# Kernel tuning notes

Measured on AMD Instinct MI355X. Metric: run time of the kernel, lower is better.

## Reference

```python
import jax, jax.numpy as jnp
import numpy as np
from jax import lax

EPS = 1e-8  # torch CosineSimilarity eps
TAU = 0.5   # temperature

def _l2norm(v):
    # clamp norm like torch.nn.CosineSimilarity
    n = jnp.sqrt(jnp.sum(v * v, axis=-1, keepdims=True))
    return v / jnp.maximum(n, EPS)

def setup_inputs() -> dict:
    key = jax.random.key(0)
    k1, k2, k3, k4 = jax.random.split(key, 4)
    B, C, H, W = 64, 3, 384, 384
    hidden, size, L = 768, 16, 1024
    x = jax.random.normal(k1, (B, C, H, W), dtype=jnp.float32)
    conv_w = jax.random.normal(k2, (hidden, C, size, size), dtype=jnp.float32) * 0.02
    conv_b = jax.random.normal(k3, (hidden,), dtype=jnp.float32) * 0.02
    latent = jax.random.normal(k4, (1, L, hidden), dtype=jnp.float32)
    return {"x": x, "conv_w": conv_w, "conv_b": conv_b, "latent": latent}

def reference(x, conv_w, conv_b, latent):
    B = x.shape[0]
    stride = conv_w.shape[-1]
    # patch embedding: Conv2d stride=kernel (non-overlapping patches)
    patch = lax.conv_general_dilated(
        x, conv_w, window_strides=(stride, stride), padding='VALID',
        dimension_numbers=('NCHW', 'OIHW', 'NCHW')) + conv_b[None, :, None, None]
    D = patch.shape[1]
    patch = patch.reshape(B, D, -1).transpose(0, 2, 1)  # (B, N, D)
    N = patch.shape[1]
    pn = _l2norm(patch)                                  # (B, N, D)
    # all-pairs cosine similarity via GEMM on normalized vectors
    SIM = jnp.einsum('bnd,bmd->bnm', pn, pn)             # (B, N, N)
    off_diag = 1.0 - jnp.eye(N, dtype=SIM.dtype)
    far_sum = jnp.sum(jnp.exp(SIM / TAU) * off_diag, axis=(1, 2))  # (B,)
    # patch vs latent cosine similarity
    ln = _l2norm(latent[0])                              # (L, D)
    close = jnp.einsum('bnd,ld->bnl', pn, ln)            # (B, N, L)
    close_sum = jnp.sum(jnp.exp(close / TAU), axis=(1, 2))  # (B,)
    loss = -jnp.log(close_sum / far_sum)
    return jnp.mean(loss)
```

## Files before the change

kernel.cpp:

```cpp
#include <hip/hip_runtime.h>
#include <hip/hip_bf16.h>
#include <hip/hip_fp8.h>

#define KDIM   768
#define NPATCH 576
#define NPAD   640
#define NBATCH 64
#define MROWS  36864
#define LROWS  1024

typedef __attribute__((ext_vector_type(8))) int int8v;
typedef __attribute__((ext_vector_type(4))) int int4v;
typedef __attribute__((ext_vector_type(4))) float float4v;
typedef unsigned char u8;

__device__ inline u8 f2fp8(float f) { __hip_fp8_e4m3 t(f); return (u8)t.__x; }

__device__ __forceinline__ void gload_lds16(const u8* g, u8* l) {
    __builtin_amdgcn_global_load_lds(
        (const __attribute__((address_space(1))) unsigned int*)g,
        (__attribute__((address_space(3))) unsigned int*)l, 16, 0, 0);
}

__device__ __forceinline__ void ds_read_b256(unsigned addr, int4v& lo, int4v& hi) {
    asm volatile("ds_read_b128 %0, %2\n\tds_read_b128 %1, %2 offset:16"
                 : "=&v"(lo), "=&v"(hi) : "v"(addr));
}

__global__ __launch_bounds__(256) void im2col_cast_v(const float* __restrict__ x,
                                                     u8* __restrict__ A) {
    int t = blockIdx.x * 256 + threadIdx.x;
    int row = t / 48;
    int ci = t - row * 48;
    int c = ci >> 4, i = ci & 15;
    int b = row / NPATCH;
    int p = row - b * NPATCH;
    int ph = p / 24, pw = p - ph * 24;
    const float* src = x + (((size_t)b * 3 + c) * 384 + ph * 16 + i) * 384 + pw * 16;
    float4v f[4];
#pragma unroll
    for (int q = 0; q < 4; q++) f[q] = *(const float4v*)(src + q * 4);
    unsigned int o[4];
#pragma unroll
    for (int q = 0; q < 4; q++) {
        o[q] = 0;
#pragma unroll
        for (int e = 0; e < 4; e++) o[q] |= ((unsigned int)f2fp8(f[q][e])) << (8 * e);
    }
    *(int4v*)(A + (size_t)row * KDIM + c * 256 + i * 16) = *(int4v*)o;
}

__global__ __launch_bounds__(256) void cast_w(const float* __restrict__ src,
                                              u8* __restrict__ dst) {
    int t = blockIdx.x * 256 + threadIdx.x;
    const float* s = src + (size_t)t * 16;
    unsigned int o[4];
#pragma unroll
    for (int q = 0; q < 4; q++) {
        float4v f = *(const float4v*)(s + q * 4);
        o[q] = 0;
#pragma unroll
        for (int e = 0; e < 4; e++) o[q] |= ((unsigned int)f2fp8(f[e] * 32.0f)) << (8 * e);
    }
    *(int4v*)(dst + (size_t)t * 16) = *(int4v*)o;
}

__global__ __launch_bounds__(256) void normalize_latent(const float* __restrict__ src,
                                                        u8* __restrict__ dst) {
    int wave = threadIdx.x >> 6, lane = threadIdx.x & 63;
    int row = blockIdx.x * 4 + wave;
    const float4v* pr = (const float4v*)(src + (size_t)row * KDIM);
    float4v v[3];
    float ss = 0.f;
#pragma unroll
    for (int c = 0; c < 3; c++) {
        v[c] = pr[lane + 64 * c];
#pragma unroll
        for (int e = 0; e < 4; e++) ss += v[c][e] * v[c][e];
    }
#pragma unroll
    for (int off = 32; off; off >>= 1) ss += __shfl_xor(ss, off);
    float scale = 16.0f / fmaxf(sqrtf(ss), 1e-8f);
#pragma unroll
    for (int c = 0; c < 3; c++) {
        unsigned int o = 0;
#pragma unroll
        for (int e = 0; e < 4; e++) o |= ((unsigned int)f2fp8(v[c][e] * scale)) << (8 * e);
        *(unsigned int*)(dst + (size_t)row * KDIM + c * 256 + lane * 4) = o;
    }
}

__global__ __launch_bounds__(256) void inv_norm(const float* __restrict__ rssq,
                                                float* __restrict__ rn) {
    int t = blockIdx.x * 256 + threadIdx.x;
    int p = t % NPAD;
    rn[t] = (p < NPATCH) ? (1.0f / fmaxf(sqrtf(rssq[t]), 1e-8f)) : 0.0f;
}

__device__ __forceinline__ void gemm_mainloop_fp8(const u8* __restrict__ Ab,
                                                  const u8* __restrict__ Bb,
                                                  u8* As, u8* Bs,
                                                  float4v acc[4][4], int sA, int sB) {
    int tid = threadIdx.x;
    int lane = tid & 63;
    int wu = __builtin_amdgcn_readfirstlane(tid >> 6);
    int quad = lane >> 4, l15 = lane & 15;
    int wm = wu & 1, wn = wu >> 1;
    int lr = lane >> 3, ls = lane & 7;
    int gs = ((((ls >> 1) - lr) & 3) << 1) | (ls & 1);
    int gvoff = lr * KDIM + gs * 16;
    const u8* gAu = Ab + (size_t)(wu * 32) * KDIM;
    const u8* gBu = Bb + (size_t)(wu * 32) * KDIM;
    int woffL = wu * 32 * 128;
    int lg = ((quad + (l15 & 3)) & 3) * 32;
    unsigned asb = (unsigned)(size_t)As + (unsigned)((wm * 64 + l15) * 128 + lg);
    unsigned bsb = (unsigned)(size_t)Bs + (unsigned)((wn * 64 + l15) * 128 + lg);

#pragma unroll
    for (int i = 0; i < 4; i++) {
        gload_lds16(gAu + i * 8 * KDIM + gvoff, As + woffL + i * 1024);
        gload_lds16(gBu + i * 8 * KDIM + gvoff, Bs + woffL + i * 1024);
    }
#pragma unroll 1
    for (int t = 0; t < 6; t++) {
        int cur = (t & 1) * 16384;
        if (t < 5) {
            int nxt = ((t + 1) & 1) * 16384;
            int ks = (t + 1) * 128;
#pragma unroll
            for (int i = 0; i < 4; i++) {
                gload_lds16(gAu + ks + i * 8 * KDIM + gvoff, As + nxt + woffL + i * 1024);
                gload_lds16(gBu + ks + i * 8 * KDIM + gvoff, Bs + nxt + woffL + i * 1024);
            }
            asm volatile("s_waitcnt vmcnt(8)" ::: "memory");
        } else {
            asm volatile("s_waitcnt vmcnt(0)" ::: "memory");
        }
        __builtin_amdgcn_s_barrier();
        asm volatile("" ::: "memory");
        int4v al[4], ah[4], bl[4], bh[4];
#pragma unroll
        for (int j = 0; j < 4; j++) ds_read_b256(bsb + cur + j * 2048, bl[j], bh[j]);
#pragma unroll
        for (int i = 0; i < 4; i++) ds_read_b256(asb + cur + i * 2048, al[i], ah[i]);
        asm volatile("s_waitcnt lgkmcnt(8)"
                     : "+v"(bl[0]), "+v"(bl[1]), "+v"(bl[2]), "+v"(bl[3]),
                       "+v"(bh[0]), "+v"(bh[1]), "+v"(bh[2]), "+v"(bh[3]));
        int8v b[4];
#pragma unroll
        for (int j = 0; j < 4; j++)
            b[j] = __builtin_shufflevector(bl[j], bh[j], 0, 1, 2, 3, 4, 5, 6, 7);
        asm volatile("s_waitcnt lgkmcnt(0)"
                     : "+v"(al[0]), "+v"(al[1]), "+v"(al[2]), "+v"(al[3]),
                       "+v"(ah[0]), "+v"(ah[1]), "+v"(ah[2]), "+v"(ah[3]));
        int8v a[4];
#pragma unroll
        for (int i = 0; i < 4; i++)
            a[i] = __builtin_shufflevector(al[i], ah[i], 0, 1, 2, 3, 4, 5, 6, 7);
        __builtin_amdgcn_sched_barrier(0);
        __builtin_amdgcn_s_barrier();
        asm volatile("" ::: "memory");
        __builtin_amdgcn_s_setprio(1);
#pragma unroll
        for (int i = 0; i < 4; i++)
#pragma unroll
            for (int j = 0; j < 4; j++)
                acc[i][j] = __builtin_amdgcn_mfma_scale_f32_16x16x128_f8f6f4(
                    a[i], b[j], acc[i][j], 0, 0, 0, sA, 0, sB);
        __builtin_amdgcn_s_setprio(0);
    }
}

__device__ __forceinline__ float block_reduce_sum(float s, float* red) {
#pragma unroll
    for (int off = 32; off; off >>= 1) s += __shfl_down(s, off);
    int wave = threadIdx.x >> 6, lane = threadIdx.x & 63;
    if (lane == 0) red[wave] = s;
    __syncthreads();
    return red[0] + red[1] + red[2] + red[3];
}

__global__ __launch_bounds__(256) void gemm_conv(const u8* __restrict__ A,
                                                 const u8* __restrict__ Wm,
                                                 const float* __restrict__ bias,
                                                 u8* __restrict__ pn,
                                                 float* __restrict__ rssq) {
    __shared__ u8 As[2 * 128 * 128], Bs[2 * 128 * 128];
    int xcd = blockIdx.x & 7, q = blockIdx.x >> 3;
    int mb = xcd * 36 + q / 6;
    int nb = q % 6;
    int wave = threadIdx.x >> 6, lane = threadIdx.x & 63;
    int quad = lane >> 4, l15 = lane & 15;
    int wm = wave & 1, wn = wave >> 1;
    float4v acc[4][4] = {};
    gemm_mainloop_fp8(A + (size_t)mb * 128 * KDIM, Wm + (size_t)nb * 128 * KDIM,
                      As, Bs, acc, 0x7F7F7F7F, 0x7A7A7A7A);
    float bv[4];
#pragma unroll
    for (int j = 0; j < 4; j++) bv[j] = bias[nb * 128 + wn * 64 + j * 16 + l15];
#pragma unroll
    for (int i = 0; i < 4; i++) {
#pragma unroll
        for (int r = 0; r < 4; r++) {
            int row = mb * 128 + wm * 64 + i * 16 + quad * 4 + r;
            int b = row / NPATCH;
            int prow = row + b * 64;
            float ssq = 0.f;
#pragma unroll
            for (int j = 0; j < 4; j++) {
                int col = nb * 128 + wn * 64 + j * 16 + l15;
                float v = acc[i][j][r] + bv[j];
                ssq += v * v;
                pn[(size_t)prow * KDIM + col] = f2fp8(v * 16.0f);
            }
#pragma unroll
            for (int off = 1; off < 16; off <<= 1) ssq += __shfl_xor(ssq, off);
            if (l15 == 0) atomicAdd(&rssq[prow], ssq);
        }
    }
}

__global__ __launch_bounds__(256) void gemm_scores(const u8* __restrict__ pn,
                                                   const u8* __restrict__ Lm,
                                                   const float* __restrict__ rn,
                                                   float* __restrict__ far_sum,
                                                   float* __restrict__ close_sum) {
    __shared__ u8 As[2 * 128 * 128], Bs[2 * 128 * 128];
    __shared__ float red[4];
    int wave = threadIdx.x >> 6, lane = threadIdx.x & 63;
    int quad = lane >> 4, l15 = lane & 15;
    int wm = wave & 1, wn = wave >> 1;
    float4v acc[4][4] = {};

    if (blockIdx.x < 2560) {
        int xcd = blockIdx.x & 7, q = blockIdx.x >> 3;
        int mb = xcd * 40 + (q >> 3);
        int nb = q & 7;
        gemm_mainloop_fp8(pn + (size_t)mb * 128 * KDIM, Lm + (size_t)nb * 128 * KDIM,
                          As, Bs, acc, 0x7B7B7B7B, 0x7B7B7B7B);
        int batch = mb / 5;
        int ptile = (mb - batch * 5) * 128;
        float s = 0.f;
#pragma unroll
        for (int i = 0; i < 4; i++) {
#pragma unroll
            for (int r = 0; r < 4; r++) {
                int p = ptile + wm * 64 + i * 16 + quad * 4 + r;
                if (p < NPATCH) {
                    float rrow = rn[batch * NPAD + p];
#pragma unroll
                    for (int j = 0; j < 4; j++) s += __expf(2.0f * acc[i][j][r] * rrow);
                }
            }
        }
        float tot = block_reduce_sum(s, red);
        if (threadIdx.x == 0) atomicAdd(&close_sum[batch], tot);
    } else {
        int sbid = blockIdx.x - 2560;
        int xcd = sbid & 7, q = sbid >> 3;
        int b = xcd * 8 + q / 15;
        int t = q % 15;
        int mt, nt;
        if (t < 5) { mt = t; nt = t; }
        else {
            int u = t - 5;
            mt = (u < 4) ? 0 : (u < 7) ? 1 : (u < 9) ? 2 : 3;
            nt = (u < 4) ? u + 1 : (u < 7) ? u - 2 : (u < 9) ? u - 5 : 4;
        }
        const u8* base = pn + (size_t)b * NPAD * KDIM;
        gemm_mainloop_fp8(base + (size_t)mt * 128 * KDIM, base + (size_t)nt * 128 * KDIM,
                          As, Bs, acc, 0x7B7B7B7B, 0x7B7B7B7B);
        const float* rnb = rn + b * NPAD;
        float rcol[4];
#pragma unroll
        for (int j = 0; j < 4; j++) rcol[j] = rnb[nt * 128 + wn * 64 + j * 16 + l15];
        float s = 0.f;
#pragma unroll
        for (int i = 0; i < 4; i++) {
#pragma unroll
            for (int r = 0; r < 4; r++) {
                int row = mt * 128 + wm * 64 + i * 16 + quad * 4 + r;
                if (row < NPATCH) {
                    float rrow = rnb[row];
#pragma unroll
                    for (int j = 0; j < 4; j++) {
                        int col = nt * 128 + wn * 64 + j * 16 + l15;
                        if (col < NPATCH && row != col)
                            s += __expf(2.0f * acc[i][j][r] * rrow * rcol[j]);
                    }
                }
            }
        }
        if (mt != nt) s *= 2.0f;
        float tot = block_reduce_sum(s, red);
        if (threadIdx.x == 0) atomicAdd(&far_sum[b], tot);
    }
}

__global__ void loss_kernel(const float* __restrict__ far_sum,
                            const float* __restrict__ close_sum,
                            float* __restrict__ out) {
    int t = threadIdx.x;
    float v = logf(far_sum[t]) - logf(close_sum[t]);
#pragma unroll
    for (int off = 32; off; off >>= 1) v += __shfl_xor(v, off);
    if (t == 0) out[0] = v * (1.0f / 64.0f);
}

extern "C" void kernel_launch(void* const* d_in, const int* in_sizes, int n_in,
                              void* d_out, int out_size, void* d_ws, size_t ws_size,
                              hipStream_t stream) {
    const float* x      = (const float*)d_in[0];
    const float* conv_w = (const float*)d_in[1];
    const float* conv_b = (const float*)d_in[2];
    const float* latent = (const float*)d_in[3];
    float* out = (float*)d_out;
    char* ws = (char*)d_ws;

    u8* pn = (u8*)ws;
    u8* A  = (u8*)(ws + 31457280);
    u8* Wm = (u8*)(ws + 59768832);
    u8* Lm = (u8*)(ws + 60358656);
    float* rssq = (float*)(ws + 61145088);
    float* sums = (float*)(ws + 61308928);
    float* rn   = (float*)(ws + 31457280);
    float* far_sum = sums;
    float* close_sum = sums + 64;

    hipMemsetAsync(rssq, 0, (40960 + 128) * sizeof(float), stream);
    im2col_cast_v<<<36864 * 48 / 256, 256, 0, stream>>>(x, A);
    cast_w<<<144, 256, 0, stream>>>(conv_w, Wm);
    normalize_latent<<<LROWS / 4, 256, 0, stream>>>(latent, Lm);

    gemm_conv<<<288 * 6, 256, 0, stream>>>(A, Wm, conv_b, pn, rssq);
    inv_norm<<<160, 256, 0, stream>>>(rssq, rn);

    gemm_scores<<<2560 + 960, 256, 0, stream>>>(pn, Lm, rn, far_sum, close_sum);

    loss_kernel<<<1, 64, 0, stream>>>(far_sum, close_sum, out);
}
```

Before: 291.4 us.

## Widen GEMM tiles to 128x256 with 512-thread blocks and new LDS swizzle

Both FP8 GEMM kernels move from 128x128 tiles on 256 threads to 128x256 tiles on 512 threads. Each A tile is now reused across twice as many output columns, which cuts global and LDS traffic per FLOP. The LDS swizzle is changed to an 8-way 16-byte pattern with separate low and high read addresses. The far-sum tiling now enumerates upper-triangular 128x256 tiles per batch, weighting each half-tile by 0, 1 or 2. This adds more LDS per block and more complex tile indexing, and may lower occupancy.

After: 311.7 us. 6.9% more time.

```diff
diff --git a/kernel.cpp b/kernel.cpp
--- a/kernel.cpp
+++ b/kernel.cpp
@@ -22,10 +22,8 @@
         (__attribute__((address_space(3))) unsigned int*)l, 16, 0, 0);
 }
 
-__device__ __forceinline__ void ds_read_b256(unsigned addr, int4v& lo, int4v& hi) {
-    asm volatile("ds_read_b128 %0, %2\n\tds_read_b128 %1, %2 offset:16"
-                 : "=&v"(lo), "=&v"(hi) : "v"(addr));
-}
+#define DSR(dst, areg, imm) \
+    asm volatile("ds_read_b128 %0, %1 offset:" #imm : "=&v"(dst) : "v"(areg))
 
 __global__ __launch_bounds__(256) void im2col_cast_v(const float* __restrict__ x,
                                                      u8* __restrict__ A) {
@@ -107,42 +105,57 @@
     int quad = lane >> 4, l15 = lane & 15;
     int wm = wu & 1, wn = wu >> 1;
     int lr = lane >> 3, ls = lane & 7;
-    int gs = ((((ls >> 1) - lr) & 3) << 1) | (ls & 1);
+    int gs = (ls - lr) & 7;
     int gvoff = lr * KDIM + gs * 16;
-    const u8* gAu = Ab + (size_t)(wu * 32) * KDIM;
+    const u8* gAu = Ab + (size_t)(wu * 16) * KDIM;
     const u8* gBu = Bb + (size_t)(wu * 32) * KDIM;
-    int woffL = wu * 32 * 128;
-    int lg = ((quad + (l15 & 3)) & 3) * 32;
-    unsigned asb = (unsigned)(size_t)As + (unsigned)((wm * 64 + l15) * 128 + lg);
-    unsigned bsb = (unsigned)(size_t)Bs + (unsigned)((wn * 64 + l15) * 128 + lg);
-
-#pragma unroll
-    for (int i = 0; i < 4; i++) {
-        gload_lds16(gAu + i * 8 * KDIM + gvoff, As + woffL + i * 1024);
-        gload_lds16(gBu + i * 8 * KDIM + gvoff, Bs + woffL + i * 1024);
-    }
+    int woffA = wu * 16 * 128;
+    int woffB = wu * 32 * 128;
+    int pl = ((2 * quad) + (l15 & 7)) & 7;
+    int ph = ((2 * quad + 1) + (l15 & 7)) & 7;
+    unsigned asbL = (unsigned)(size_t)As + (unsigned)((wm * 64 + l15) * 128 + pl * 16);
+    unsigned asbH = (unsigned)(size_t)As + (unsigned)((wm * 64 + l15) * 128 + ph * 16);
+    unsigned bsbL = (unsigned)(size_t)Bs + (unsigned)((wn * 64 + l15) * 128 + pl * 16);
+    unsigned bsbH = (unsigned)(size_t)Bs + (unsigned)((wn * 64 + l15) * 128 + ph * 16);
+
+#pragma unroll
+    for (int i = 0; i < 2; i++)
+        gload_lds16(gAu + i * 8 * KDIM + gvoff, As + woffA + i * 1024);
+#pragma unroll
+    for (int i = 0; i < 4; i++)
+        gload_lds16(gBu + i * 8 * KDIM + gvoff, Bs + woffB + i * 1024);
+
 #pragma unroll 1
     for (int t = 0; t < 6; t++) {
-        int cur = (t & 1) * 16384;
+        int curA = (t & 1) * 16384;
+        int curB = (t & 1) * 32768;
         if (t < 5) {
-            int nxt = ((t + 1) & 1) * 16384;
+            int nxtA = ((t + 1) & 1) * 16384;
+            int nxtB = ((t + 1) & 1) * 32768;
             int ks = (t + 1) * 128;
 #pragma unroll
-            for (int i = 0; i < 4; i++) {
-                gload_lds16(gAu + ks + i * 8 * KDIM + gvoff, As + nxt + woffL + i * 1024);
-                gload_lds16(gBu + ks + i * 8 * KDIM + gvoff, Bs + nxt + woffL + i * 1024);
-            }
-            asm volatile("s_waitcnt vmcnt(8)" ::: "memory");
+            for (int i = 0; i < 2; i++)
+                gload_lds16(gAu + ks + i * 8 * KDIM + gvoff, As + nxtA + woffA + i * 1024);
+#pragma unroll
+            for (int i = 0; i < 4; i++)
+                gload_lds16(gBu + ks + i * 8 * KDIM + gvoff, Bs + nxtB + woffB + i * 1024);
+            asm volatile("s_waitcnt vmcnt(6)" ::: "memory");
         } else {
             asm volatile("s_waitcnt vmcnt(0)" ::: "memory");
         }
         __builtin_amdgcn_s_barrier();
         asm volatile("" ::: "memory");
+        unsigned aL = asbL + curA, aH = asbH + curA;
+        unsigned bL = bsbL + curB, bH = bsbH + curB;
         int4v al[4], ah[4], bl[4], bh[4];
-#pragma unroll
-        for (int j = 0; j < 4; j++) ds_read_b256(bsb + cur + j * 2048, bl[j], bh[j]);
-#pragma unroll
-        for (int i = 0; i < 4; i++) ds_read_b256(asb + cur + i * 2048, al[i], ah[i]);
+        DSR(bl[0], bL, 0);    DSR(bh[0], bH, 0);
+        DSR(bl[1], bL, 2048); DSR(bh[1], bH, 2048);
+        DSR(bl[2], bL, 4096); DSR(bh[2], bH, 4096);
+        DSR(bl[3], bL, 6144); DSR(bh[3], bH, 6144);
+        DSR(al[0], aL, 0);    DSR(ah[0], aH, 0);
+        DSR(al[1], aL, 2048); DSR(ah[1], aH, 2048);
+        DSR(al[2], aL, 4096); DSR(ah[2], aH, 4096);
+        DSR(al[3], aL, 6144); DSR(ah[3], aH, 6144);
         asm volatile("s_waitcnt lgkmcnt(8)"
                      : "+v"(bl[0]), "+v"(bl[1]), "+v"(bl[2]), "+v"(bl[3]),
                        "+v"(bh[0]), "+v"(bh[1]), "+v"(bh[2]), "+v"(bh[3]));
@@ -177,27 +190,30 @@
     int wave = threadIdx.x >> 6, lane = threadIdx.x & 63;
     if (lane == 0) red[wave] = s;
     __syncthreads();
-    return red[0] + red[1] + red[2] + red[3];
-}
-
-__global__ __launch_bounds__(256) void gemm_conv(const u8* __restrict__ A,
+    float tot = 0.f;
+#pragma unroll
+    for (int w = 0; w < 8; w++) tot += red[w];
+    return tot;
+}
+
+__global__ __launch_bounds__(512) void gemm_conv(const u8* __restrict__ A,
                                                  const u8* __restrict__ Wm,
                                                  const float* __restrict__ bias,
                                                  u8* __restrict__ pn,
                                                  float* __restrict__ rssq) {
-    __shared__ u8 As[2 * 128 * 128], Bs[2 * 128 * 128];
+    __shared__ u8 As[2 * 128 * 128], Bs[2 * 256 * 128];
     int xcd = blockIdx.x & 7, q = blockIdx.x >> 3;
-    int mb = xcd * 36 + q / 6;
-    int nb = q % 6;
+    int mb = xcd * 36 + q / 3;
+    int nb = q % 3;
     int wave = threadIdx.x >> 6, lane = threadIdx.x & 63;
     int quad = lane >> 4, l15 = lane & 15;
     int wm = wave & 1, wn = wave >> 1;
     float4v acc[4][4] = {};
-    gemm_mainloop_fp8(A + (size_t)mb * 128 * KDIM, Wm + (size_t)nb * 128 * KDIM,
+    gemm_mainloop_fp8(A + (size_t)mb * 128 * KDIM, Wm + (size_t)nb * 256 * KDIM,
                       As, Bs, acc, 0x7F7F7F7F, 0x7A7A7A7A);
     float bv[4];
 #pragma unroll
-    for (int j = 0; j < 4; j++) bv[j] = bias[nb * 128 + wn * 64 + j * 16 + l15];
+    for (int j = 0; j < 4; j++) bv[j] = bias[nb * 256 + wn * 64 + j * 16 + l15];
 #pragma unroll
     for (int i = 0; i < 4; i++) {
 #pragma unroll
@@ -208,7 +224,7 @@
             float ssq = 0.f;
 #pragma unroll
             for (int j = 0; j < 4; j++) {
-                int col = nb * 128 + wn * 64 + j * 16 + l15;
+                int col = nb * 256 + wn * 64 + j * 16 + l15;
                 float v = acc[i][j][r] + bv[j];
                 ssq += v * v;
                 pn[(size_t)prow * KDIM + col] = f2fp8(v * 16.0f);
@@ -220,23 +236,23 @@
     }
 }
 
-__global__ __launch_bounds__(256) void gemm_scores(const u8* __restrict__ pn,
+__global__ __launch_bounds__(512) void gemm_scores(const u8* __restrict__ pn,
                                                    const u8* __restrict__ Lm,
                                                    const float* __restrict__ rn,
                                                    float* __restrict__ far_sum,
                                                    float* __restrict__ close_sum) {
-    __shared__ u8 As[2 * 128 * 128], Bs[2 * 128 * 128];
-    __shared__ float red[4];
+    __shared__ u8 As[2 * 128 * 128], Bs[2 * 256 * 128];
+    __shared__ float red[8];
     int wave = threadIdx.x >> 6, lane = threadIdx.x & 63;
     int quad = lane >> 4, l15 = lane & 15;
     int wm = wave & 1, wn = wave >> 1;
     float4v acc[4][4] = {};
 
-    if (blockIdx.x < 2560) {
+    if (blockIdx.x < 1280) {
         int xcd = blockIdx.x & 7, q = blockIdx.x >> 3;
-        int mb = xcd * 40 + (q >> 3);
-        int nb = q & 7;
-        gemm_mainloop_fp8(pn + (size_t)mb * 128 * KDIM, Lm + (size_t)nb * 128 * KDIM,
+        int mb = xcd * 40 + (q >> 2);
+        int nb = q & 3;
+        gemm_mainloop_fp8(pn + (size_t)mb * 128 * KDIM, Lm + (size_t)nb * 256 * KDIM,
                           As, Bs, acc, 0x7B7B7B7B, 0x7B7B7B7B);
         int batch = mb / 5;
         int ptile = (mb - batch * 5) * 128;
@@ -256,24 +272,25 @@
         float tot = block_reduce_sum(s, red);
         if (threadIdx.x == 0) atomicAdd(&close_sum[batch], tot);
     } else {
-        int sbid = blockIdx.x - 2560;
-        int xcd = sbid & 7, q = sbid >> 3;
-        int b = xcd * 8 + q / 15;
-        int t = q % 15;
-        int mt, nt;
-        if (t < 5) { mt = t; nt = t; }
-        else {
-            int u = t - 5;
-            mt = (u < 4) ? 0 : (u < 7) ? 1 : (u < 9) ? 2 : 3;
-            nt = (u < 4) ? u + 1 : (u < 7) ? u - 2 : (u < 9) ? u - 5 : 4;
-        }
+        int sbid = blockIdx.x - 1280;
+        int xcd = sbid & 7, qq = sbid >> 3;
+        int b = xcd * 8 + qq / 11;
+        int idx = qq % 11;
+        int mt = (idx < 3) ? 0 : (idx < 6) ? 1 : (idx < 8) ? 2 : (idx < 10) ? 3 : 4;
+        int t2 = (idx < 3) ? idx : (idx < 6) ? idx - 3 : (idx < 8) ? idx - 5
+                                 : (idx < 10) ? idx - 7 : 2;
         const u8* base = pn + (size_t)b * NPAD * KDIM;
-        gemm_mainloop_fp8(base + (size_t)mt * 128 * KDIM, base + (size_t)nt * 128 * KDIM,
+        gemm_mainloop_fp8(base + (size_t)mt * 128 * KDIM, base + (size_t)t2 * 256 * KDIM,
                           As, Bs, acc, 0x7B7B7B7B, 0x7B7B7B7B);
         const float* rnb = rn + b * NPAD;
+        int nt128 = t2 * 2 + (wn >> 1);
+        float w = (nt128 < mt) ? 0.0f : (nt128 == mt) ? 1.0f : 2.0f;
         float rcol[4];
 #pragma unroll
-        for (int j = 0; j < 4; j++) rcol[j] = rnb[nt * 128 + wn * 64 + j * 16 + l15];
+        for (int j = 0; j < 4; j++) {
+            int col = t2 * 256 + wn * 64 + j * 16 + l15;
+            rcol[j] = (col < NPATCH) ? rnb[col] : 0.0f;
+        }
         float s = 0.f;
 #pragma unroll
         for (int i = 0; i < 4; i++) {
@@ -284,14 +301,14 @@
                     float rrow = rnb[row];
 #pragma unroll
                     for (int j = 0; j < 4; j++) {
-                        int col = nt * 128 + wn * 64 + j * 16 + l15;
+                        int col = t2 * 256 + wn * 64 + j * 16 + l15;
                         if (col < NPATCH && row != col)
                             s += __expf(2.0f * acc[i][j][r] * rrow * rcol[j]);
                     }
                 }
             }
         }
-        if (mt != nt) s *= 2.0f;
+        s *= w;
         float tot = block_reduce_sum(s, red);
         if (threadIdx.x == 0) atomicAdd(&far_sum[b], tot);
     }
@@ -332,10 +349,10 @@
     cast_w<<<144, 256, 0, stream>>>(conv_w, Wm);
     normalize_latent<<<LROWS / 4, 256, 0, stream>>>(latent, Lm);
 
-    gemm_conv<<<288 * 6, 256, 0, stream>>>(A, Wm, conv_b, pn, rssq);
+    gemm_conv<<<288 * 3, 512, 0, stream>>>(A, Wm, conv_b, pn, rssq);
     inv_norm<<<160, 256, 0, stream>>>(rssq, rn);
 
-    gemm_scores<<<2560 + 960, 256, 0, stream>>>(pn, Lm, rn, far_sum, close_sum);
+    gemm_scores<<<1280 + 704, 512, 0, stream>>>(pn, Lm, rn, far_sum, close_sum);
 
     loss_kernel<<<1, 64, 0, stream>>>(far_sum, close_sum, out);
 }
```
